# Performance work log

Measured on AMD Instinct MI355X. Metric: run time of the kernel, lower is better.

## Reference

```python
import jax, jax.numpy as jnp
import numpy as np

N_NODES = 50000
N_EDGES = 800000
DIM = 128
N_LAYERS = 2          # num_layers - 1 GIN layers
NUM_GRAPHS = 512      # rows of the sparse graph_pool matrix
BN_EPS = 1e-5


def setup_inputs() -> dict:
    key = jax.random.key(0)
    ks = jax.random.split(key, 10)
    x = jax.random.normal(ks[0], (N_NODES, DIM), dtype=jnp.float32)
    edge_src = jax.random.randint(ks[1], (N_EDGES,), 0, N_NODES, dtype=jnp.int32)
    edge_dst = jax.random.randint(ks[2], (N_EDGES,), 0, N_NODES, dtype=jnp.int32)
    edge_weight = jax.random.uniform(ks[3], (N_EDGES,), dtype=jnp.float32)
    graph_ids = jnp.sort(jax.random.randint(ks[4], (N_NODES,), 0, NUM_GRAPHS, dtype=jnp.int32))
    pool_w = jnp.ones((N_NODES,), dtype=jnp.float32)
    scale = 1.0 / np.sqrt(DIM)
    W1 = jax.random.normal(ks[5], (N_LAYERS, DIM, DIM), dtype=jnp.float32) * scale
    b1 = jnp.zeros((N_LAYERS, DIM), dtype=jnp.float32)
    W2 = jax.random.normal(ks[6], (N_LAYERS, DIM, DIM), dtype=jnp.float32) * scale
    b2 = jnp.zeros((N_LAYERS, DIM), dtype=jnp.float32)
    bn_gamma = jnp.ones((N_LAYERS, DIM), dtype=jnp.float32)
    bn_beta = jnp.zeros((N_LAYERS, DIM), dtype=jnp.float32)
    return {"x": x, "edge_src": edge_src, "edge_dst": edge_dst,
            "edge_weight": edge_weight, "graph_ids": graph_ids, "pool_w": pool_w,
            "W1": W1, "b1": b1, "W2": W2, "b2": b2,
            "bn_gamma": bn_gamma, "bn_beta": bn_beta}


def reference(x, edge_src, edge_dst, edge_weight, graph_ids, pool_w,
              W1, b1, W2, b2, bn_gamma, bn_beta):
    h = x
    n = h.shape[0]
    for l in range(N_LAYERS):
        # pooled = adj @ h, adj in COO form: adj[dst, src] = edge_weight
        msg = edge_weight[:, None] * h[edge_src]                    # [E, D] gather
        pooled = jax.ops.segment_sum(msg, edge_dst, num_segments=n) # [N, D] scatter-add
        # 2-linear MLP (num_mlp_layers=2): Linear -> ReLU -> Linear
        hid = jax.nn.relu(pooled @ W1[l] + b1[l])
        z = hid @ W2[l] + b2[l]
        # BatchNorm1d over the node dimension (training-mode batch stats)
        mu = jnp.mean(z, axis=0)
        var = jnp.mean(jnp.square(z - mu), axis=0)
        z = bn_gamma[l] * (z - mu) * jax.lax.rsqrt(var + BN_EPS) + bn_beta[l]
        h = jax.nn.relu(z)
    x_nodes = h
    # pooled_x = graph_pool @ h, graph_pool[g, i] = pool_w[i] for node i in graph g
    pooled_x = jax.ops.segment_sum(pool_w[:, None] * h, graph_ids,
                                   num_segments=NUM_GRAPHS)
    return pooled_x, x_nodes
```

## Files before the change

kernel.cpp:

```cpp
#include <hip/hip_runtime.h>

#define N_NODES    50000
#define N_EDGES    800000
#define DIM        128
#define NUM_GRAPHS 512
#define BN_EPS     1e-5f

#define NBUCK      196
#define CAP        4608
#define NBINS      2048
#define TILE       4096
#define MLP_ROWS   128
#define POOL_SPLIT 4

typedef unsigned int u32;
typedef unsigned short u16;
typedef __attribute__((ext_vector_type(8))) short bf16x8;
typedef __attribute__((ext_vector_type(4))) float f32x4;

__device__ __forceinline__ u16 f2bf(float f) {
    u32 u = __float_as_uint(f);
    u += 0x7FFF + ((u >> 16) & 1);
    return (u16)(u >> 16);
}
__device__ __forceinline__ float bf2f(u16 h) {
    return __uint_as_float((u32)h << 16);
}

__global__ __launch_bounds__(256)
void prep_kernel(const float* __restrict__ x, const float* __restrict__ W1,
                 const float* __restrict__ W2, u16* __restrict__ hx,
                 u16* __restrict__ wt, float* __restrict__ zreg,
                 float* __restrict__ out_pool)
{
    if (blockIdx.x < 256) {
        int idx = blockIdx.x * 256 + threadIdx.x;
        int m    = idx >> 14;
        int f    = idx & 16383;
        int c    = (f >> 11) & 7;
        int kk   = (f >> 9) & 3;
        int lane = (f >> 3) & 63;
        int e    = f & 7;
        int k = kk * 32 + ((lane >> 4) << 3) + e;
        int j = c * 16 + (lane & 15);
        const float* src = (m & 1) ? W2 : W1;
        src += (m >> 1) * 128 * 128;
        wt[idx] = f2bf(src[k * 128 + j]);
    } else if (blockIdx.x < 1280) {
        const long long n4 = (long long)N_NODES * DIM / 4;
        long long stride = 1024LL * 256;
        for (long long i = (blockIdx.x - 256) * 256LL + threadIdx.x; i < n4; i += stride) {
            float4 v = ((const float4*)x)[i];
            ushort4 o;
            o.x = f2bf(v.x); o.y = f2bf(v.y); o.z = f2bf(v.z); o.w = f2bf(v.w);
            ((ushort4*)hx)[i] = o;
        }
    } else {
        int stride = 64 * 256;
        for (int i = (blockIdx.x - 1280) * 256 + threadIdx.x;
             i < 768 + NUM_GRAPHS * DIM; i += stride) {
            if (i < 768) zreg[i] = 0.f;
            else         out_pool[i - 768] = 0.f;
        }
    }
}

__global__ __launch_bounds__(512)
void partitionA(const int* __restrict__ src, const int* __restrict__ dst,
                const float* __restrict__ ew, int* __restrict__ gCursor,
                uint2* __restrict__ ed2)
{
    __shared__ int cnt[NBUCK];
    __shared__ int off[NBUCK];
    __shared__ int gb[NBUCK];
    __shared__ u32 stg_sw[TILE];
    __shared__ u32 stg_d[TILE];
    __shared__ int scanb[256];

    const int t = threadIdx.x;
    const int base = blockIdx.x * TILE;
    const int tcnt = min(TILE, N_EDGES - base);

    if (t < NBUCK) cnt[t] = 0;
    __syncthreads();

    u32 swv[8], dv[8];
    int rk[8], bk[8];
    #pragma unroll
    for (int j = 0; j < 8; ++j) {
        int e = base + j * 512 + t;
        if (e < N_EDGES) {
            int d = dst[e];
            swv[j] = ((u32)f2bf(ew[e]) << 16) | (u32)src[e];
            dv[j]  = (u32)d;
            bk[j]  = d >> 8;
            rk[j]  = atomicAdd(&cnt[bk[j]], 1);
        } else bk[j] = -1;
    }
    __syncthreads();

    {
        int v = (t < NBUCK) ? cnt[t] : 0;
        if (t < 256) scanb[t] = v;
        __syncthreads();
        for (int o = 1; o < 256; o <<= 1) {
            int x = (t < 256 && t >= o) ? scanb[t - o] : 0;
            __syncthreads();
            if (t < 256) scanb[t] += x;
            __syncthreads();
        }
        if (t < NBUCK) off[t] = scanb[t] - v;
    }
    __syncthreads();

    #pragma unroll
    for (int j = 0; j < 8; ++j) {
        if (bk[j] >= 0) {
            int idx = off[bk[j]] + rk[j];
            stg_sw[idx] = swv[j];
            stg_d[idx]  = dv[j];
        }
    }
    if (t < NBUCK && cnt[t] > 0) gb[t] = atomicAdd(&gCursor[t], cnt[t]);
    __syncthreads();

    for (int j = t; j < tcnt; j += 512) {
        u32 d = stg_d[j];
        int b = (int)(d >> 8);
        long long pos = (long long)b * CAP + gb[b] + (j - off[b]);
        ed2[pos] = make_uint2(stg_sw[j], d);
    }
}

__global__ __launch_bounds__(256)
void partitionB(const uint2* __restrict__ ed2, const int* __restrict__ gCursor,
                int* __restrict__ rowptr, u32* __restrict__ ed)
{
    __shared__ int bstart[256];
    __shared__ int hist[NBINS];
    __shared__ int cursor[NBINS];
    __shared__ int sc[256];

    const int b = blockIdx.x;
    const int t = threadIdx.x;

    {
        int v = (t < NBUCK) ? gCursor[t] : 0;
        sc[t] = v;
        __syncthreads();
        for (int o = 1; o < 256; o <<= 1) {
            int x = (t >= o) ? sc[t - o] : 0;
            __syncthreads();
            sc[t] += x;
            __syncthreads();
        }
        bstart[t] = sc[t] - v;
    }
    __syncthreads();

    const int s0 = bstart[b];
    const int n  = gCursor[b];
    const uint2* srcp = ed2 + (long long)b * CAP;

    #pragma unroll
    for (int q = 0; q < 8; ++q) hist[t + q * 256] = 0;
    __syncthreads();
    for (int j = t; j < n; j += 256) {
        uint2 r = srcp[j];
        int bin = (int)((r.y & 255u) << 3) | (int)((r.x & 0xFFFFu) >> 13);
        atomicAdd(&hist[bin], 1);
    }
    __syncthreads();

    int loc[8]; int sum = 0;
    #pragma unroll
    for (int q = 0; q < 8; ++q) { loc[q] = hist[t * 8 + q]; sum += loc[q]; }
    sc[t] = sum;
    __syncthreads();
    for (int o = 1; o < 256; o <<= 1) {
        int x = (t >= o) ? sc[t - o] : 0;
        __syncthreads();
        sc[t] += x;
        __syncthreads();
    }
    int run = sc[t] - sum;
    rowptr[b * 256 + t] = s0 + run;
    #pragma unroll
    for (int q = 0; q < 8; ++q) {
        cursor[t * 8 + q] = s0 + run;
        run += loc[q];
    }
    __syncthreads();

    for (int j = t; j < n; j += 256) {
        uint2 r = srcp[j];
        int bin = (int)((r.y & 255u) << 3) | (int)((r.x & 0xFFFFu) >> 13);
        int p = atomicAdd(&cursor[bin], 1);
        ed[p] = r.x;
    }
}

template<bool BN>
__global__ __launch_bounds__(256)
void gather_spmm(const u16* __restrict__ h, const u32* __restrict__ ed,
                 const int* __restrict__ rowptr, u16* __restrict__ pooled,
                 const float* __restrict__ stats, const float* __restrict__ gamma,
                 const float* __restrict__ beta)
{
    __shared__ float scs[128];
    __shared__ float shs[128];
    if (BN) {
        if (threadIdx.x < 128) {
            int c = threadIdx.x;
            float mu  = stats[c] * (1.f / N_NODES);
            float var = stats[128 + c] * (1.f / N_NODES) - mu * mu;
            float s   = gamma[c] * rsqrtf(var + BN_EPS);
            scs[c] = s;
            shs[c] = beta[c] - mu * s;
        }
        __syncthreads();
    }

    int node = blockIdx.x * 16 + (threadIdx.x >> 4);
    int lane = threadIdx.x & 15;
    int beg = rowptr[node];
    int end = rowptr[node + 1];

    float sc8[8], sh8[8];
    if (BN) {
        #pragma unroll
        for (int q = 0; q < 8; ++q) {
            sc8[q] = scs[lane * 8 + q];
            sh8[q] = shs[lane * 8 + q];
        }
    }

    float acc[8];
    #pragma unroll
    for (int q = 0; q < 8; ++q) acc[q] = 0.f;

    u32 sw_cur = (beg + lane < end) ? ed[beg + lane] : 0u;
    for (int base = beg; base < end; base += 16) {
        u32 sw_next = (base + 16 + lane < end) ? ed[base + 16 + lane] : 0u;
        int cnt = min(16, end - base);
        #pragma unroll 4
        for (int i = 0; i < cnt; ++i) {
            u32 rec = __shfl(sw_cur, i, 16);
            long long s = (long long)(rec & 0xFFFFu);
            float w = bf2f((u16)(rec >> 16));
            bf16x8 hv = *((const bf16x8*)(h + (s << 7)) + lane);
            #pragma unroll
            for (int q = 0; q < 8; ++q) {
                float v = bf2f((u16)hv[q]);
                if (BN) v = fmaxf(v * sc8[q] + sh8[q], 0.f);
                acc[q] += w * v;
            }
        }
        sw_cur = sw_next;
    }
    bf16x8 o;
    #pragma unroll
    for (int q = 0; q < 8; ++q) o[q] = (short)f2bf(acc[q]);
    *((bf16x8*)(pooled + ((long long)node << 7)) + lane) = o;
}

__global__ __launch_bounds__(512)
void fused_mlp(const u16* __restrict__ A, const u16* __restrict__ wtL,
               const float* __restrict__ b1, const float* __restrict__ b2,
               u16* __restrict__ Z, float* __restrict__ stats)
{
    __shared__ __align__(16) u16 wfrag[32768];
    __shared__ float ssum[128];
    __shared__ float ssq[128];

    const int tid  = threadIdx.x;
    const int lane = tid & 63;
    const int wave = tid >> 6;
    const int l15  = lane & 15;
    const int lk   = lane >> 4;
    const int row0 = blockIdx.x * MLP_ROWS;
    const int wrow = wave * 16;

    #pragma unroll
    for (int i = 0; i < 8; ++i) {
        int idx = tid + i * 512;
        *(bf16x8*)&wfrag[idx * 8] = *(const bf16x8*)(wtL + idx * 8);
    }
    if (tid < 128) { ssum[tid] = 0.f; ssq[tid] = 0.f; }

    bf16x8 afr[4];
    {
        int rg = row0 + wrow + l15;
        bool ok = rg < N_NODES;
        const u16* ap = A + (long long)rg * 128 + lk * 8;
        bf16x8 zero = {};
        #pragma unroll
        for (int kk = 0; kk < 4; ++kk)
            afr[kk] = ok ? *(const bf16x8*)(ap + kk * 32) : zero;
    }
    __syncthreads();

    f32x4 acc1[8];
    #pragma unroll
    for (int c = 0; c < 8; ++c) {
        float bv = b1[c * 16 + l15];
        f32x4 a = {bv, bv, bv, bv};
        #pragma unroll
        for (int kk = 0; kk < 4; ++kk) {
            bf16x8 w = *(bf16x8*)&wfrag[((c * 4 + kk) * 64 + lane) * 8];
            a = __builtin_amdgcn_mfma_f32_16x16x32_bf16(afr[kk], w, a, 0, 0, 0);
        }
        acc1[c] = a;
    }
    __syncthreads();

    #pragma unroll
    for (int c = 0; c < 8; ++c) {
        #pragma unroll
        for (int i = 0; i < 4; ++i) {
            int row = wrow + lk * 4 + i;
            int col = c * 16 + l15;
            wfrag[row * 128 + (col ^ ((row & 15) << 3))] = f2bf(fmaxf(acc1[c][i], 0.f));
        }
    }

    bf16x8 afr2[4];
    {
        int row = wrow + l15;
        #pragma unroll
        for (int kk = 0; kk < 4; ++kk)
            afr2[kk] = *(bf16x8*)&wfrag[row * 128 + ((kk * 32 + lk * 8) ^ ((row & 15) << 3))];
    }

    #pragma unroll
    for (int c = 0; c < 8; ++c) {
        float bv = b2[c * 16 + l15];
        f32x4 a = {bv, bv, bv, bv};
        #pragma unroll
        for (int kk = 0; kk < 4; ++kk) {
            bf16x8 w = *(bf16x8*)&wfrag[16384 + ((c * 4 + kk) * 64 + lane) * 8];
            a = __builtin_amdgcn_mfma_f32_16x16x32_bf16(afr2[kk], w, a, 0, 0, 0);
        }
        float s = 0.f, sq = 0.f;
        #pragma unroll
        for (int i = 0; i < 4; ++i) {
            int row = wrow + lk * 4 + i;
            int rg  = row0 + row;
            float v = a[i];
            bool ok = rg < N_NODES;
            if (ok) { s += v; sq += v * v; }
            wfrag[row * 128 + ((c * 16 + l15) ^ ((row & 15) << 3))] = ok ? f2bf(v) : (u16)0;
        }
        s  += __shfl_xor(s, 16);  s  += __shfl_xor(s, 32);
        sq += __shfl_xor(sq, 16); sq += __shfl_xor(sq, 32);
        if (lk == 0) {
            atomicAdd(&ssum[c * 16 + l15], s);
            atomicAdd(&ssq[c * 16 + l15], sq);
        }
    }

    #pragma unroll
    for (int j = 0; j < 4; ++j) {
        int chunk = j * 64 + lane;
        int rl  = chunk >> 4;
        int c8  = chunk & 15;
        int row = wrow + rl;
        int rg  = row0 + row;
        if (rg < N_NODES) {
            bf16x8 v = *(bf16x8*)&wfrag[row * 128 + ((c8 * 8) ^ ((row & 15) << 3))];
            *(bf16x8*)(Z + (long long)rg * 128 + c8 * 8) = v;
        }
    }
    __syncthreads();
    if (tid < 128) {
        atomicAdd(&stats[tid], ssum[tid]);
        atomicAdd(&stats[128 + tid], ssq[tid]);
    }
}

__global__ __launch_bounds__(256)
void graph_pool_bn(const u16* __restrict__ z, const float* __restrict__ stats,
                   const float* __restrict__ gamma, const float* __restrict__ beta,
                   const int* __restrict__ gid, const float* __restrict__ pw,
                   float* __restrict__ out_nodes, float* __restrict__ out_pool)
{
    __shared__ float scs[128];
    __shared__ float shs[128];
    if (threadIdx.x < 128) {
        int c = threadIdx.x;
        float mu  = stats[c] * (1.f / N_NODES);
        float var = stats[128 + c] * (1.f / N_NODES) - mu * mu;
        float s   = gamma[c] * rsqrtf(var + BN_EPS);
        scs[c] = s;
        shs[c] = beta[c] - mu * s;
    }
    __syncthreads();

    int g    = blockIdx.x >> 2;
    int part = blockIdx.x & 3;

    int lo = 0, hi = N_NODES;
    while (lo < hi) { int m = (lo + hi) >> 1; if (gid[m] < g) lo = m + 1; else hi = m; }
    int start = lo;
    hi = N_NODES;
    while (lo < hi) { int m = (lo + hi) >> 1; if (gid[m] < g + 1) lo = m + 1; else hi = m; }
    int end = lo;

    int len  = end - start;
    int qlen = (len + 3) >> 2;
    int s = start + part * qlen;
    int e = min(end, s + qlen);

    const int t  = threadIdx.x;
    const int rg = t >> 5;
    const int c4 = t & 31;
    float4 sc4 = *(float4*)&scs[c4 * 4];
    float4 sh4 = *(float4*)&shs[c4 * 4];

    float4 acc = make_float4(0.f, 0.f, 0.f, 0.f);
    for (int r = s + rg; r < e; r += 8) {
        float w = pw[r];
        ushort4 hv = *((const ushort4*)(z + (long long)r * DIM) + c4);
        float4 v;
        v.x = fmaxf(bf2f(hv.x) * sc4.x + sh4.x, 0.f);
        v.y = fmaxf(bf2f(hv.y) * sc4.y + sh4.y, 0.f);
        v.z = fmaxf(bf2f(hv.z) * sc4.z + sh4.z, 0.f);
        v.w = fmaxf(bf2f(hv.w) * sc4.w + sh4.w, 0.f);
        *((float4*)(out_nodes + (long long)r * DIM) + c4) = v;
        acc.x += w * v.x; acc.y += w * v.y;
        acc.z += w * v.z; acc.w += w * v.w;
    }

    __shared__ float4 sd[256];
    sd[t] = acc;
    __syncthreads();
    if (t < 32) {
        float4 tot = sd[t];
        #pragma unroll
        for (int i = 1; i < 8; ++i) {
            float4 v = sd[i * 32 + t];
            tot.x += v.x; tot.y += v.y; tot.z += v.z; tot.w += v.w;
        }
        float* op = out_pool + g * DIM + t * 4;
        atomicAdd(op + 0, tot.x);
        atomicAdd(op + 1, tot.y);
        atomicAdd(op + 2, tot.z);
        atomicAdd(op + 3, tot.w);
    }
}

extern "C" void kernel_launch(void* const* d_in, const int* in_sizes, int n_in,
                              void* d_out, int out_size, void* d_ws, size_t ws_size,
                              hipStream_t stream)
{
    const float* x    = (const float*)d_in[0];
    const int*   esrc = (const int*)d_in[1];
    const int*   edst = (const int*)d_in[2];
    const float* ew   = (const float*)d_in[3];
    const int*   gid  = (const int*)d_in[4];
    const float* pw   = (const float*)d_in[5];
    const float* W1   = (const float*)d_in[6];
    const float* b1   = (const float*)d_in[7];
    const float* W2   = (const float*)d_in[8];
    const float* b2   = (const float*)d_in[9];
    const float* gam  = (const float*)d_in[10];
    const float* bet  = (const float*)d_in[11];

    float* out_pool  = (float*)d_out;
    float* out_nodes = (float*)d_out + NUM_GRAPHS * DIM;

    const size_t NF = (size_t)N_NODES * DIM;
    char* w = (char*)d_ws;
    u32*   ed       = (u32*)w;        w += (size_t)N_EDGES * sizeof(u32);
    u16*   pooledBf = (u16*)w;        w += NF * sizeof(u16);
    u16*   zBf      = (u16*)w;        w += NF * sizeof(u16);
    u16*   hx       = (u16*)w;        w += NF * sizeof(u16);
    u16*   wt       = (u16*)w;        w += (size_t)4 * 128 * 128 * sizeof(u16);
    float* stats0   = (float*)w;      w += 256 * sizeof(float);
    float* stats1   = (float*)w;      w += 256 * sizeof(float);
    int*   gCursor  = (int*)w;        w += 256 * sizeof(int);
    int*   rowptr   = (int*)w;        w += (NBUCK * 256 + 64) * sizeof(int);

    uint2* ed2cap   = (uint2*)pooledBf;

    const int mlpGrid    = (N_NODES + MLP_ROWS - 1) / MLP_ROWS;
    const int gatherGrid = (N_NODES + 15) / 16;
    const int partGrid   = (N_EDGES + TILE - 1) / TILE;

    prep_kernel<<<1344, 256, 0, stream>>>(x, W1, W2, hx, wt, stats0, out_pool);
    partitionA<<<partGrid, 512, 0, stream>>>(esrc, edst, ew, gCursor, ed2cap);
    partitionB<<<NBUCK, 256, 0, stream>>>(ed2cap, gCursor, rowptr, ed);

    gather_spmm<false><<<gatherGrid, 256, 0, stream>>>(hx, ed, rowptr, pooledBf,
                                                       nullptr, nullptr, nullptr);
    fused_mlp<<<mlpGrid, 512, 0, stream>>>(pooledBf, wt, b1, b2, zBf, stats0);

    gather_spmm<true><<<gatherGrid, 256, 0, stream>>>(zBf, ed, rowptr, pooledBf,
                                                      stats0, gam, bet);
    fused_mlp<<<mlpGrid, 512, 0, stream>>>(pooledBf, wt + 32768,
                                           b1 + DIM, b2 + DIM, zBf, stats1);

    graph_pool_bn<<<NUM_GRAPHS * POOL_SPLIT, 256, 0, stream>>>(
        zBf, stats1, gam + DIM, bet + DIM, gid, pw, out_nodes, out_pool);
}
```

Baseline: 152.8 us.

## Fuse bf16 prep with edge partition pass and widen partitionB to 512 threads

Merges the x/weight bf16 conversion and zero-fill work into the same launch as the first edge-bucketing pass, using block-index ranges so that independent jobs run side by side instead of back to back. Because the bucketing pass now runs concurrently with the zero-fill, the global bucket cursors are cleared by a separate tiny kernel launched beforehand. partitionB moves to 512 threads with 4 histogram bins per thread and a 512-wide scan, aiming to shorten the per-bucket sort. The cost is a larger mixed-role kernel whose shared-memory footprint applies to every block, plus longer scan loops in partitionB.

```diff
diff --git a/kernel.cpp b/kernel.cpp
--- a/kernel.cpp
+++ b/kernel.cpp
@@ -13,6 +13,12 @@
 #define MLP_ROWS   128
 #define POOL_SPLIT 4
 
+#define RA_N       196
+#define RX_N       512
+#define RW_N       128
+#define RZ_N       32
+#define RTOTAL     (RA_N + RX_N + RW_N + RZ_N)
+
 typedef unsigned int u32;
 typedef unsigned short u16;
 typedef __attribute__((ext_vector_type(8))) short bf16x8;
@@ -28,13 +34,94 @@
 }
 
 __global__ __launch_bounds__(256)
-void prep_kernel(const float* __restrict__ x, const float* __restrict__ W1,
-                 const float* __restrict__ W2, u16* __restrict__ hx,
-                 u16* __restrict__ wt, float* __restrict__ zreg,
-                 float* __restrict__ out_pool)
-{
-    if (blockIdx.x < 256) {
-        int idx = blockIdx.x * 256 + threadIdx.x;
+void fill_cursor_kernel(int* __restrict__ gCursor)
+{
+    gCursor[threadIdx.x] = 0;
+}
+
+__global__ __launch_bounds__(512)
+void prep_partA(const float* __restrict__ x, const float* __restrict__ W1,
+                const float* __restrict__ W2, const int* __restrict__ src,
+                const int* __restrict__ dst, const float* __restrict__ ew,
+                u16* __restrict__ hx, u16* __restrict__ wt,
+                float* __restrict__ zreg, float* __restrict__ out_pool,
+                int* __restrict__ gCursor, uint2* __restrict__ ed2)
+{
+    __shared__ __align__(16) char smem[36992];
+
+    const int t = threadIdx.x;
+
+    if (blockIdx.x < RA_N) {
+        int* cnt   = (int*)smem;
+        int* off   = cnt + NBUCK;
+        int* gb    = off + NBUCK;
+        int* scanb = gb + NBUCK;
+        u32* stg_sw = (u32*)(scanb + 256);
+        u32* stg_d  = stg_sw + TILE;
+
+        const int base = blockIdx.x * TILE;
+        const int tcnt = min(TILE, N_EDGES - base);
+
+        if (t < NBUCK) cnt[t] = 0;
+        __syncthreads();
+
+        u32 swv[8], dv[8];
+        int rk[8], bk[8];
+        #pragma unroll
+        for (int j = 0; j < 8; ++j) {
+            int e = base + j * 512 + t;
+            if (e < N_EDGES) {
+                int d = dst[e];
+                swv[j] = ((u32)f2bf(ew[e]) << 16) | (u32)src[e];
+                dv[j]  = (u32)d;
+                bk[j]  = d >> 8;
+                rk[j]  = atomicAdd(&cnt[bk[j]], 1);
+            } else bk[j] = -1;
+        }
+        __syncthreads();
+
+        {
+            int v = (t < NBUCK) ? cnt[t] : 0;
+            if (t < 256) scanb[t] = v;
+            __syncthreads();
+            for (int o = 1; o < 256; o <<= 1) {
+                int xv = (t < 256 && t >= o) ? scanb[t - o] : 0;
+                __syncthreads();
+                if (t < 256) scanb[t] += xv;
+                __syncthreads();
+            }
+            if (t < NBUCK) off[t] = scanb[t] - v;
+        }
+        __syncthreads();
+
+        #pragma unroll
+        for (int j = 0; j < 8; ++j) {
+            if (bk[j] >= 0) {
+                int idx = off[bk[j]] + rk[j];
+                stg_sw[idx] = swv[j];
+                stg_d[idx]  = dv[j];
+            }
+        }
+        if (t < NBUCK && cnt[t] > 0) gb[t] = atomicAdd(&gCursor[t], cnt[t]);
+        __syncthreads();
+
+        for (int j = t; j < tcnt; j += 512) {
+            u32 d = stg_d[j];
+            int b = (int)(d >> 8);
+            long long pos = (long long)b * CAP + gb[b] + (j - off[b]);
+            ed2[pos] = make_uint2(stg_sw[j], d);
+        }
+    } else if (blockIdx.x < RA_N + RX_N) {
+        const long long n4 = (long long)N_NODES * DIM / 4;
+        long long stride = (long long)RX_N * 512;
+        for (long long i = (blockIdx.x - RA_N) * 512LL + t; i < n4; i += stride) {
+            float4 v = ((const float4*)x)[i];
+            ushort4 o;
+            o.x = f2bf(v.x); o.y = f2bf(v.y); o.z = f2bf(v.z); o.w = f2bf(v.w);
+            ((ushort4*)hx)[i] = o;
+        }
+    } else if (blockIdx.x < RA_N + RX_N + RW_N) {
+        int idx = (blockIdx.x - RA_N - RX_N) * 512 + t;
         int m    = idx >> 14;
         int f    = idx & 16383;
         int c    = (f >> 11) & 7;
@@ -43,156 +130,76 @@
         int e    = f & 7;
         int k = kk * 32 + ((lane >> 4) << 3) + e;
         int j = c * 16 + (lane & 15);
-        const float* src = (m & 1) ? W2 : W1;
-        src += (m >> 1) * 128 * 128;
-        wt[idx] = f2bf(src[k * 128 + j]);
-    } else if (blockIdx.x < 1280) {
-        const long long n4 = (long long)N_NODES * DIM / 4;
-        long long stride = 1024LL * 256;
-        for (long long i = (blockIdx.x - 256) * 256LL + threadIdx.x; i < n4; i += stride) {
-            float4 v = ((const float4*)x)[i];
-            ushort4 o;
-            o.x = f2bf(v.x); o.y = f2bf(v.y); o.z = f2bf(v.z); o.w = f2bf(v.w);
-            ((ushort4*)hx)[i] = o;
-        }
+        const float* srcw = (m & 1) ? W2 : W1;
+        srcw += (m >> 1) * 128 * 128;
+        wt[idx] = f2bf(srcw[k * 128 + j]);
     } else {
-        int stride = 64 * 256;
-        for (int i = (blockIdx.x - 1280) * 256 + threadIdx.x;
-             i < 768 + NUM_GRAPHS * DIM; i += stride) {
-            if (i < 768) zreg[i] = 0.f;
-            else         out_pool[i - 768] = 0.f;
+        int stride = RZ_N * 512;
+        for (int i = (blockIdx.x - RA_N - RX_N - RW_N) * 512 + t;
+             i < 512 + NUM_GRAPHS * DIM; i += stride) {
+            if (i < 512) zreg[i] = 0.f;
+            else         out_pool[i - 512] = 0.f;
         }
     }
 }
 
 __global__ __launch_bounds__(512)
-void partitionA(const int* __restrict__ src, const int* __restrict__ dst,
-                const float* __restrict__ ew, int* __restrict__ gCursor,
-                uint2* __restrict__ ed2)
-{
-    __shared__ int cnt[NBUCK];
-    __shared__ int off[NBUCK];
-    __shared__ int gb[NBUCK];
-    __shared__ u32 stg_sw[TILE];
-    __shared__ u32 stg_d[TILE];
-    __shared__ int scanb[256];
-
-    const int t = threadIdx.x;
-    const int base = blockIdx.x * TILE;
-    const int tcnt = min(TILE, N_EDGES - base);
-
-    if (t < NBUCK) cnt[t] = 0;
-    __syncthreads();
-
-    u32 swv[8], dv[8];
-    int rk[8], bk[8];
-    #pragma unroll
-    for (int j = 0; j < 8; ++j) {
-        int e = base + j * 512 + t;
-        if (e < N_EDGES) {
-            int d = dst[e];
-            swv[j] = ((u32)f2bf(ew[e]) << 16) | (u32)src[e];
-            dv[j]  = (u32)d;
-            bk[j]  = d >> 8;
-            rk[j]  = atomicAdd(&cnt[bk[j]], 1);
-        } else bk[j] = -1;
-    }
-    __syncthreads();
-
-    {
-        int v = (t < NBUCK) ? cnt[t] : 0;
-        if (t < 256) scanb[t] = v;
-        __syncthreads();
-        for (int o = 1; o < 256; o <<= 1) {
-            int x = (t < 256 && t >= o) ? scanb[t - o] : 0;
-            __syncthreads();
-            if (t < 256) scanb[t] += x;
-            __syncthreads();
-        }
-        if (t < NBUCK) off[t] = scanb[t] - v;
-    }
-    __syncthreads();
-
-    #pragma unroll
-    for (int j = 0; j < 8; ++j) {
-        if (bk[j] >= 0) {
-            int idx = off[bk[j]] + rk[j];
-            stg_sw[idx] = swv[j];
-            stg_d[idx]  = dv[j];
-        }
-    }
-    if (t < NBUCK && cnt[t] > 0) gb[t] = atomicAdd(&gCursor[t], cnt[t]);
-    __syncthreads();
-
-    for (int j = t; j < tcnt; j += 512) {
-        u32 d = stg_d[j];
-        int b = (int)(d >> 8);
-        long long pos = (long long)b * CAP + gb[b] + (j - off[b]);
-        ed2[pos] = make_uint2(stg_sw[j], d);
-    }
-}
-
-__global__ __launch_bounds__(256)
 void partitionB(const uint2* __restrict__ ed2, const int* __restrict__ gCursor,
                 int* __restrict__ rowptr, u32* __restrict__ ed)
 {
-    __shared__ int bstart[256];
+    __shared__ int sc2[512];
     __shared__ int hist[NBINS];
     __shared__ int cursor[NBINS];
-    __shared__ int sc[256];
 
     const int b = blockIdx.x;
     const int t = threadIdx.x;
 
-    {
-        int v = (t < NBUCK) ? gCursor[t] : 0;
-        sc[t] = v;
-        __syncthreads();
-        for (int o = 1; o < 256; o <<= 1) {
-            int x = (t >= o) ? sc[t - o] : 0;
-            __syncthreads();
-            sc[t] += x;
-            __syncthreads();
-        }
-        bstart[t] = sc[t] - v;
-    }
-    __syncthreads();
-
-    const int s0 = bstart[b];
+    int v = (t < NBUCK) ? gCursor[t] : 0;
+    sc2[t] = v;
+    __syncthreads();
+    for (int o = 1; o < 512; o <<= 1) {
+        int xv = (t >= o) ? sc2[t - o] : 0;
+        __syncthreads();
+        sc2[t] += xv;
+        __syncthreads();
+    }
     const int n  = gCursor[b];
+    const int s0 = sc2[b] - n;
+    __syncthreads();
+
     const uint2* srcp = ed2 + (long long)b * CAP;
 
     #pragma unroll
-    for (int q = 0; q < 8; ++q) hist[t + q * 256] = 0;
-    __syncthreads();
-    for (int j = t; j < n; j += 256) {
+    for (int q = 0; q < 4; ++q) hist[t + q * 512] = 0;
+    __syncthreads();
+    for (int j = t; j < n; j += 512) {
         uint2 r = srcp[j];
         int bin = (int)((r.y & 255u) << 3) | (int)((r.x & 0xFFFFu) >> 13);
         atomicAdd(&hist[bin], 1);
     }
     __syncthreads();
 
-    int loc[8]; int sum = 0;
-    #pragma unroll
-    for (int q = 0; q < 8; ++q) { loc[q] = hist[t * 8 + q]; sum += loc[q]; }
-    sc[t] = sum;
-    __syncthreads();
-    for (int o = 1; o < 256; o <<= 1) {
-        int x = (t >= o) ? sc[t - o] : 0;
-        __syncthreads();
-        sc[t] += x;
-        __syncthreads();
-    }
-    int run = sc[t] - sum;
-    rowptr[b * 256 + t] = s0 + run;
-    #pragma unroll
-    for (int q = 0; q < 8; ++q) {
-        cursor[t * 8 + q] = s0 + run;
+    int loc[4]; int sum = 0;
+    #pragma unroll
+    for (int q = 0; q < 4; ++q) { loc[q] = hist[t * 4 + q]; sum += loc[q]; }
+    sc2[t] = sum;
+    __syncthreads();
+    for (int o = 1; o < 512; o <<= 1) {
+        int xv = (t >= o) ? sc2[t - o] : 0;
+        __syncthreads();
+        sc2[t] += xv;
+        __syncthreads();
+    }
+    int run = sc2[t] - sum;
+    if ((t & 1) == 0) rowptr[b * 256 + (t >> 1)] = s0 + run;
+    #pragma unroll
+    for (int q = 0; q < 4; ++q) {
+        cursor[t * 4 + q] = s0 + run;
         run += loc[q];
     }
     __syncthreads();
 
-    for (int j = t; j < n; j += 256) {
+    for (int j = t; j < n; j += 512) {
         uint2 r = srcp[j];
         int bin = (int)((r.y & 255u) << 3) | (int)((r.x & 0xFFFFu) >> 13);
         int p = atomicAdd(&cursor[bin], 1);
@@ -485,11 +492,12 @@
 
     const int mlpGrid    = (N_NODES + MLP_ROWS - 1) / MLP_ROWS;
     const int gatherGrid = (N_NODES + 15) / 16;
-    const int partGrid   = (N_EDGES + TILE - 1) / TILE;
-
-    prep_kernel<<<1344, 256, 0, stream>>>(x, W1, W2, hx, wt, stats0, out_pool);
-    partitionA<<<partGrid, 512, 0, stream>>>(esrc, edst, ew, gCursor, ed2cap);
-    partitionB<<<NBUCK, 256, 0, stream>>>(ed2cap, gCursor, rowptr, ed);
+
+    fill_cursor_kernel<<<1, 256, 0, stream>>>(gCursor);
+    prep_partA<<<RTOTAL, 512, 0, stream>>>(x, W1, W2, esrc, edst, ew,
+                                           hx, wt, stats0, out_pool,
+                                           gCursor, ed2cap);
+    partitionB<<<NBUCK, 512, 0, stream>>>(ed2cap, gCursor, rowptr, ed);
 
     gather_spmm<false><<<gatherGrid, 256, 0, stream>>>(hx, ed, rowptr, pooledBf,
                                                        nullptr, nullptr, nullptr);
```

Measured after the change: 152.7 us (median of 2 runs). No clear change (-0.0%).
